# Optimization experiments

Measured on AMD Instinct MI355X. Metric: run time of the kernel, lower is better.

## Reference

```python
import jax, jax.numpy as jnp
import numpy as np

H = 512      # n_lstm_hidden (hardcoded in module)
ATTN = 256   # n_attn_hidden (hardcoded in module)


def setup_inputs() -> dict:
    key = jax.random.key(0)
    ks = jax.random.split(key, 10)
    seq_len, teams, nt = 16, 16, 64
    na = teams * 8
    bs = seq_len * nt
    return {
        "x": jax.random.normal(ks[0], (seq_len, teams, 16), jnp.float32),
        "hxs": jax.random.normal(ks[1], (bs, na, H), jnp.float32),
        "cxs": jax.random.normal(ks[2], (bs, na, H), jnp.float32),
        "h_self": jax.random.normal(ks[3], (bs, na, H), jnp.float32),
        "h_inter": jax.random.normal(ks[4], (bs, na, ATTN), jnp.float32),
        "reset": jax.random.randint(ks[5], (bs, 1), 0, 2, jnp.int32),
        "W_ih": jax.random.normal(ks[6], (4 * H, H), jnp.float32) * 0.02,
        "W_hh": jax.random.normal(ks[7], (4 * H, H), jnp.float32) * 0.02,
        "b_ih": jnp.zeros((4 * H,), jnp.float32),
        "b_hh": jnp.zeros((4 * H,), jnp.float32),
    }


def reference(x, hxs, cxs, h_self, h_inter, reset, W_ih, W_hh, b_ih, b_hh):
    seq_len, teams = x.shape[0], x.shape[1]
    na = teams * 8
    bs = h_self.shape[0]
    nt = bs // seq_len

    # LSTM input: tail half of self features concatenated with inter features -> (bs, na, H)
    h = jnp.concatenate([h_self[:, :, ATTN:], h_inter], axis=-1)
    # (bs, na, H) -> (seq_len, nt*na, H), matching view(nt,seq,na,-1).transpose(1,0)
    h_seq = h.reshape(nt, seq_len, na, H).transpose(1, 0, 2, 3).reshape(seq_len, nt * na, H)

    # per-step keep mask: resets[i::seq_len] == reset.reshape(nt, seq_len)[:, i]
    m = 1.0 - reset.astype(h.dtype).reshape(nt, seq_len).T          # (seq_len, nt)
    m_seq = jnp.broadcast_to(m[:, :, None], (seq_len, nt, na)).reshape(seq_len, nt * na, 1)

    # initial state from each trajectory start: hxs[::seq_len]
    h0 = hxs[::seq_len].reshape(nt * na, H)
    c0 = cxs[::seq_len].reshape(nt * na, H)

    def step(carry, inp):
        hp, cp = carry
        xt, mt = inp
        hp = hp * mt
        cp = cp * mt
        gates = xt @ W_ih.T + b_ih + hp @ W_hh.T + b_hh
        i, f, g, o = jnp.split(gates, 4, axis=-1)
        c = jax.nn.sigmoid(f) * cp + jax.nn.sigmoid(i) * jnp.tanh(g)
        hn = jax.nn.sigmoid(o) * jnp.tanh(c)
        return (hn, c), (hn, c)

    _, (hys, cys) = jax.lax.scan(step, (h0, c0), (h_seq, m_seq))

    def fold(y):
        # (seq_len, nt*na, H) -> transpose to (nt, seq, na, H) contiguous,
        # then torch .view(seq_len, nt, -1) reinterpretation == reshape here
        return y.reshape(seq_len, nt, na, H).transpose(1, 0, 2, 3).reshape(seq_len, nt, na * H)

    hys_out = fold(hys)
    cys_out = fold(cys)
    return (hys_out, cys_out)
```

## Files before the change

kernel.cpp:

```cpp
#include <hip/hip_runtime.h>

typedef __attribute__((ext_vector_type(8))) short bf16x8;
typedef __attribute__((ext_vector_type(16))) float f32x16;

#define SEQ  16
#define NAG  128
#define HD   512

__device__ __forceinline__ unsigned short f2bf(float x) {
  unsigned int u = __float_as_uint(x);
  return (unsigned short)((u + 0x7fffu + ((u >> 16) & 1u)) >> 16);
}
__device__ __forceinline__ float sigm(float x) { return 1.0f / (1.0f + __expf(-x)); }
__device__ __forceinline__ float tanh_(float x) { return 2.0f / (1.0f + __expf(-2.0f * x)) - 1.0f; }

__global__ void prep_pack(const float* __restrict__ Wih, const float* __restrict__ Whh,
                          const float* __restrict__ bih, const float* __restrict__ bhh,
                          unsigned short* __restrict__ Wpk, float* __restrict__ bsum) {
  const int t  = blockIdx.x >> 6;
  const int ks = blockIdx.x & 63;
  const int l  = threadIdx.x;
  const int n  = t * 32 + (l & 31);
  const int k  = ks * 16 + (l >> 5) * 8;
  const float* p = (k < 512) ? (Wih + (size_t)n * 512 + k) : (Whh + (size_t)n * 512 + (k - 512));
  float4 w0 = *reinterpret_cast<const float4*>(p);
  float4 w1 = *reinterpret_cast<const float4*>(p + 4);
  bf16x8 v = {(short)f2bf(w0.x), (short)f2bf(w0.y), (short)f2bf(w0.z), (short)f2bf(w0.w),
              (short)f2bf(w1.x), (short)f2bf(w1.y), (short)f2bf(w1.z), (short)f2bf(w1.w)};
  *reinterpret_cast<bf16x8*>(Wpk + ((size_t)blockIdx.x * 64 + l) * 8) = v;
  if (ks == 0 && l < 32) bsum[n] = bih[n] + bhh[n];
}

template <bool PACKED>
__device__ __forceinline__ bf16x8 loadB(const unsigned short* __restrict__ Wpk,
                                        const float* __restrict__ Wih,
                                        const float* __restrict__ Whh,
                                        int tile, int ks, int lane) {
  if (PACKED) {
    return *reinterpret_cast<const bf16x8*>(Wpk + (((size_t)tile * 64 + ks) * 64 + lane) * 8);
  } else {
    int n = tile * 32 + (lane & 31);
    int k = ks * 16 + (lane >> 5) * 8;
    const float* p = (k < 512) ? (Wih + (size_t)n * 512 + k) : (Whh + (size_t)n * 512 + (k - 512));
    float4 w0 = *reinterpret_cast<const float4*>(p);
    float4 w1 = *reinterpret_cast<const float4*>(p + 4);
    return bf16x8{(short)f2bf(w0.x), (short)f2bf(w0.y), (short)f2bf(w0.z), (short)f2bf(w0.w),
                  (short)f2bf(w1.x), (short)f2bf(w1.y), (short)f2bf(w1.z), (short)f2bf(w1.w)};
  }
}

template <bool PACKED>
__global__ __launch_bounds__(512, 2)
void lstm32(const float* __restrict__ hxs, const float* __restrict__ cxs,
            const float* __restrict__ h_self, const float* __restrict__ h_inter,
            const int* __restrict__ reset,
            const unsigned short* __restrict__ Wpk, const float* __restrict__ bsum,
            const float* __restrict__ Wih, const float* __restrict__ Whh,
            const float* __restrict__ bih, const float* __restrict__ bhh,
            float* __restrict__ out) {
  __shared__ __align__(16) unsigned short x_lds[32 * 512];
  __shared__ __align__(16) unsigned short h_lds[2][32 * 512];

  const int tid  = threadIdx.x;
  const int w    = tid >> 6;
  const int lane = tid & 63;
  const int colB = lane & 31;
  const int khB  = lane >> 5;
  const int row  = colB;
  const int asw  = (row & 7) << 3;

  const int bid    = blockIdx.x;
  const int traj   = bid >> 2;
  const int agent0 = (bid & 3) * 32;

  const int rS  = tid >> 4;
  const int l16 = tid & 15;
  const int swS = (rS & 7) << 3;

  const size_t CYS = (size_t)SEQ * 64 * NAG * HD;

  {
    const float* src = hxs + ((size_t)traj * SEQ * NAG + (agent0 + rS)) * HD;
    #pragma unroll
    for (int p = 0; p < 8; ++p) {
      int k = p * 64 + l16 * 4;
      float4 v = *reinterpret_cast<const float4*>(src + k);
      ushort4 u4 = make_ushort4(f2bf(v.x), f2bf(v.y), f2bf(v.z), f2bf(v.w));
      *reinterpret_cast<ushort4*>(&h_lds[0][rS * 512 + (k ^ swS)]) = u4;
    }
  }

  float c_reg[2][16];
  float biasv[2][4];
  {
    #pragma unroll
    for (int u = 0; u < 2; ++u)
      #pragma unroll
      for (int q = 0; q < 4; ++q) {
        int n = q * 512 + w * 64 + u * 32 + colB;
        biasv[u][q] = PACKED ? bsum[n] : (bih[n] + bhh[n]);
      }
    const size_t cbase = ((size_t)traj * SEQ * NAG + agent0) * HD;
    #pragma unroll
    for (int u = 0; u < 2; ++u)
      #pragma unroll
      for (int reg = 0; reg < 16; ++reg) {
        int r  = (reg & 3) + 8 * (reg >> 2) + 4 * khB;
        int hd = w * 64 + u * 32 + colB;
        c_reg[u][reg] = cxs[cbase + (size_t)r * HD + hd];
      }
  }

  for (int t = 0; t < SEQ; ++t) {
    const int b  = traj * SEQ + t;
    const int mt = 1 - reset[b];
    const unsigned short* hcur = h_lds[t & 1];
    unsigned short*       hnxt = h_lds[(t & 1) ^ 1];

    {
      const float* srcs = h_self  + ((size_t)b * NAG + (agent0 + rS)) * HD + 256;
      const float* srci = h_inter + ((size_t)b * NAG + (agent0 + rS)) * 256;
      #pragma unroll
      for (int p = 0; p < 8; ++p) {
        int k = p * 64 + l16 * 4;
        const float* sp = (k < 256) ? (srcs + k) : (srci + (k - 256));
        float4 v = *reinterpret_cast<const float4*>(sp);
        ushort4 u4 = make_ushort4(f2bf(v.x), f2bf(v.y), f2bf(v.z), f2bf(v.w));
        *reinterpret_cast<ushort4*>(&x_lds[rS * 512 + (k ^ swS)]) = u4;
      }
      if (mt == 0) {
        uint4* pz = (uint4*)h_lds[t & 1];
        #pragma unroll
        for (int i = 0; i < 4; ++i) pz[tid + i * 512] = uint4{0, 0, 0, 0};
      }
    }
    __syncthreads();

    auto lda = [&](int ks) -> bf16x8 {
      int kk = (ks & 31) * 16 + khB * 8;
      const unsigned short* src = (ks < 32) ? x_lds : hcur;
      return *reinterpret_cast<const bf16x8*>(src + row * 512 + (kk ^ asw));
    };

    #pragma unroll
    for (int u = 0; u < 2; ++u) {
      const int t0 = 0 * 16 + w * 2 + u, t1 = 1 * 16 + w * 2 + u,
                t2 = 2 * 16 + w * 2 + u, t3 = 3 * 16 + w * 2 + u;
      f32x16 acc[4];
      #pragma unroll
      for (int q = 0; q < 4; ++q)
        #pragma unroll
        for (int e = 0; e < 16; ++e) acc[q][e] = 0.0f;

      bf16x8 Ba[4], Bb[4];
      Ba[0] = loadB<PACKED>(Wpk, Wih, Whh, t0, 0, lane);
      Ba[1] = loadB<PACKED>(Wpk, Wih, Whh, t1, 0, lane);
      Ba[2] = loadB<PACKED>(Wpk, Wih, Whh, t2, 0, lane);
      Ba[3] = loadB<PACKED>(Wpk, Wih, Whh, t3, 0, lane);
      Bb[0] = loadB<PACKED>(Wpk, Wih, Whh, t0, 1, lane);
      Bb[1] = loadB<PACKED>(Wpk, Wih, Whh, t1, 1, lane);
      Bb[2] = loadB<PACKED>(Wpk, Wih, Whh, t2, 1, lane);
      Bb[3] = loadB<PACKED>(Wpk, Wih, Whh, t3, 1, lane);

      #pragma unroll 1
      for (int kp = 0; kp < 32; ++kp) {
        const int ks0 = kp * 2;
        bf16x8 a0 = lda(ks0);
        __builtin_amdgcn_s_setprio(1);
        acc[0] = __builtin_amdgcn_mfma_f32_32x32x16_bf16(a0, Ba[0], acc[0], 0, 0, 0);
        acc[1] = __builtin_amdgcn_mfma_f32_32x32x16_bf16(a0, Ba[1], acc[1], 0, 0, 0);
        acc[2] = __builtin_amdgcn_mfma_f32_32x32x16_bf16(a0, Ba[2], acc[2], 0, 0, 0);
        acc[3] = __builtin_amdgcn_mfma_f32_32x32x16_bf16(a0, Ba[3], acc[3], 0, 0, 0);
        __builtin_amdgcn_s_setprio(0);
        const int ksn0 = (ks0 + 2 < 64) ? ks0 + 2 : 63;
        Ba[0] = loadB<PACKED>(Wpk, Wih, Whh, t0, ksn0, lane);
        Ba[1] = loadB<PACKED>(Wpk, Wih, Whh, t1, ksn0, lane);
        Ba[2] = loadB<PACKED>(Wpk, Wih, Whh, t2, ksn0, lane);
        Ba[3] = loadB<PACKED>(Wpk, Wih, Whh, t3, ksn0, lane);
        bf16x8 a1 = lda(ks0 + 1);
        __builtin_amdgcn_s_setprio(1);
        acc[0] = __builtin_amdgcn_mfma_f32_32x32x16_bf16(a1, Bb[0], acc[0], 0, 0, 0);
        acc[1] = __builtin_amdgcn_mfma_f32_32x32x16_bf16(a1, Bb[1], acc[1], 0, 0, 0);
        acc[2] = __builtin_amdgcn_mfma_f32_32x32x16_bf16(a1, Bb[2], acc[2], 0, 0, 0);
        acc[3] = __builtin_amdgcn_mfma_f32_32x32x16_bf16(a1, Bb[3], acc[3], 0, 0, 0);
        __builtin_amdgcn_s_setprio(0);
        const int ksn1 = (ks0 + 3 < 64) ? ks0 + 3 : 63;
        Bb[0] = loadB<PACKED>(Wpk, Wih, Whh, t0, ksn1, lane);
        Bb[1] = loadB<PACKED>(Wpk, Wih, Whh, t1, ksn1, lane);
        Bb[2] = loadB<PACKED>(Wpk, Wih, Whh, t2, ksn1, lane);
        Bb[3] = loadB<PACKED>(Wpk, Wih, Whh, t3, ksn1, lane);
      }

      const int hd = w * 64 + u * 32 + colB;
      #pragma unroll
      for (int reg = 0; reg < 16; ++reg) {
        float gi = acc[0][reg] + biasv[u][0];
        float gf = acc[1][reg] + biasv[u][1];
        float gg = acc[2][reg] + biasv[u][2];
        float go = acc[3][reg] + biasv[u][3];
        float cp = mt ? c_reg[u][reg] : 0.0f;
        float cn = sigm(gf) * cp + sigm(gi) * tanh_(gg);
        float hn = sigm(go) * tanh_(cn);
        c_reg[u][reg] = cn;
        int r = (reg & 3) + 8 * (reg >> 2) + 4 * khB;
        size_t ob = ((size_t)b * NAG + agent0 + r) * HD + hd;
        out[ob] = hn;
        out[CYS + ob] = cn;
        hnxt[r * 512 + (hd ^ ((r & 7) << 3))] = f2bf(hn);
      }
    }
    __syncthreads();
  }
}

extern "C" void kernel_launch(void* const* d_in, const int* in_sizes, int n_in,
                              void* d_out, int out_size, void* d_ws, size_t ws_size,
                              hipStream_t stream) {
  (void)in_sizes; (void)n_in; (void)out_size;
  const float* hxs     = (const float*)d_in[1];
  const float* cxs     = (const float*)d_in[2];
  const float* h_self  = (const float*)d_in[3];
  const float* h_inter = (const float*)d_in[4];
  const int*   reset   = (const int*)d_in[5];
  const float* Wih     = (const float*)d_in[6];
  const float* Whh     = (const float*)d_in[7];
  const float* bih     = (const float*)d_in[8];
  const float* bhh     = (const float*)d_in[9];
  float* out = (float*)d_out;

  const size_t needW = (size_t)2048 * 1024 * sizeof(unsigned short);
  const size_t need  = needW + 2048 * sizeof(float);

  if (d_ws != nullptr && ws_size >= need) {
    unsigned short* Wpk = (unsigned short*)d_ws;
    float* bsum = (float*)((char*)d_ws + needW);
    prep_pack<<<4096, 64, 0, stream>>>(Wih, Whh, bih, bhh, Wpk, bsum);
    lstm32<true><<<256, 512, 0, stream>>>(hxs, cxs, h_self, h_inter, reset,
                                          Wpk, bsum, Wih, Whh, bih, bhh, out);
  } else {
    lstm32<false><<<256, 512, 0, stream>>>(hxs, cxs, h_self, h_inter, reset,
                                           nullptr, nullptr, Wih, Whh, bih, bhh, out);
  }
}
```

Baseline: 998.4 us.

## Double block to 16 waves, each owning one column tile per gate

Blocks grow from 512 to 1024 threads. Each of 16 waves now computes one 32-column tile for all four gates, instead of 8 waves each looping over two tiles. The bias is folded into the accumulator initialisation, and the LDS swizzle is widened to cover all 32 rows. This halves the serial MFMA chain per wave and adds more waves to hide weight-load latency, at the cost of register pressure from the aggressive launch bounds hint.

```diff
diff --git a/kernel.cpp b/kernel.cpp
--- a/kernel.cpp
+++ b/kernel.cpp
@@ -3,9 +3,9 @@
 typedef __attribute__((ext_vector_type(8))) short bf16x8;
 typedef __attribute__((ext_vector_type(16))) float f32x16;
 
-#define SEQ  16
-#define NAG  128
-#define HD   512
+#define SEQ 16
+#define NAG 128
+#define HD  512
 
 __device__ __forceinline__ unsigned short f2bf(float x) {
   unsigned int u = __float_as_uint(x);
@@ -32,32 +32,27 @@
 }
 
 template <bool PACKED>
-__device__ __forceinline__ bf16x8 loadB(const unsigned short* __restrict__ Wpk,
-                                        const float* __restrict__ Wih,
-                                        const float* __restrict__ Whh,
-                                        int tile, int ks, int lane) {
-  if (PACKED) {
-    return *reinterpret_cast<const bf16x8*>(Wpk + (((size_t)tile * 64 + ks) * 64 + lane) * 8);
-  } else {
-    int n = tile * 32 + (lane & 31);
-    int k = ks * 16 + (lane >> 5) * 8;
-    const float* p = (k < 512) ? (Wih + (size_t)n * 512 + k) : (Whh + (size_t)n * 512 + (k - 512));
-    float4 w0 = *reinterpret_cast<const float4*>(p);
-    float4 w1 = *reinterpret_cast<const float4*>(p + 4);
-    return bf16x8{(short)f2bf(w0.x), (short)f2bf(w0.y), (short)f2bf(w0.z), (short)f2bf(w0.w),
-                  (short)f2bf(w1.x), (short)f2bf(w1.y), (short)f2bf(w1.z), (short)f2bf(w1.w)};
-  }
+__device__ __forceinline__ bf16x8 loadBf(const float* __restrict__ Wih,
+                                         const float* __restrict__ Whh,
+                                         int tile, int ks, int lane) {
+  int n = tile * 32 + (lane & 31);
+  int k = ks * 16 + (lane >> 5) * 8;
+  const float* p = (k < 512) ? (Wih + (size_t)n * 512 + k) : (Whh + (size_t)n * 512 + (k - 512));
+  float4 w0 = *reinterpret_cast<const float4*>(p);
+  float4 w1 = *reinterpret_cast<const float4*>(p + 4);
+  return bf16x8{(short)f2bf(w0.x), (short)f2bf(w0.y), (short)f2bf(w0.z), (short)f2bf(w0.w),
+                (short)f2bf(w1.x), (short)f2bf(w1.y), (short)f2bf(w1.z), (short)f2bf(w1.w)};
 }
 
 template <bool PACKED>
-__global__ __launch_bounds__(512, 2)
-void lstm32(const float* __restrict__ hxs, const float* __restrict__ cxs,
-            const float* __restrict__ h_self, const float* __restrict__ h_inter,
-            const int* __restrict__ reset,
-            const unsigned short* __restrict__ Wpk, const float* __restrict__ bsum,
-            const float* __restrict__ Wih, const float* __restrict__ Whh,
-            const float* __restrict__ bih, const float* __restrict__ bhh,
-            float* __restrict__ out) {
+__global__ __launch_bounds__(1024, 4)
+void lstm16w(const float* __restrict__ hxs, const float* __restrict__ cxs,
+             const float* __restrict__ h_self, const float* __restrict__ h_inter,
+             const int* __restrict__ reset,
+             const unsigned short* __restrict__ Wpk, const float* __restrict__ bsum,
+             const float* __restrict__ Wih, const float* __restrict__ Whh,
+             const float* __restrict__ bih, const float* __restrict__ bhh,
+             float* __restrict__ out) {
   __shared__ __align__(16) unsigned short x_lds[32 * 512];
   __shared__ __align__(16) unsigned short h_lds[2][32 * 512];
 
@@ -67,49 +62,47 @@
   const int colB = lane & 31;
   const int khB  = lane >> 5;
   const int row  = colB;
-  const int asw  = (row & 7) << 3;
 
   const int bid    = blockIdx.x;
   const int traj   = bid >> 2;
   const int agent0 = (bid & 3) * 32;
 
-  const int rS  = tid >> 4;
-  const int l16 = tid & 15;
-  const int swS = (rS & 7) << 3;
+  const int rS  = tid >> 5;
+  const int l32 = tid & 31;
+  const int swS = (rS & 31) << 3;
 
   const size_t CYS = (size_t)SEQ * 64 * NAG * HD;
 
   {
     const float* src = hxs + ((size_t)traj * SEQ * NAG + (agent0 + rS)) * HD;
     #pragma unroll
-    for (int p = 0; p < 8; ++p) {
-      int k = p * 64 + l16 * 4;
+    for (int p = 0; p < 4; ++p) {
+      int k = p * 128 + l32 * 4;
       float4 v = *reinterpret_cast<const float4*>(src + k);
       ushort4 u4 = make_ushort4(f2bf(v.x), f2bf(v.y), f2bf(v.z), f2bf(v.w));
       *reinterpret_cast<ushort4*>(&h_lds[0][rS * 512 + (k ^ swS)]) = u4;
     }
   }
 
-  float c_reg[2][16];
-  float biasv[2][4];
+  const int hd = w * 32 + colB;
+  float c_reg[16];
+  float biasv[4];
   {
     #pragma unroll
-    for (int u = 0; u < 2; ++u)
-      #pragma unroll
-      for (int q = 0; q < 4; ++q) {
-        int n = q * 512 + w * 64 + u * 32 + colB;
-        biasv[u][q] = PACKED ? bsum[n] : (bih[n] + bhh[n]);
-      }
+    for (int q = 0; q < 4; ++q)
+      biasv[q] = PACKED ? bsum[q * 512 + hd] : (bih[q * 512 + hd] + bhh[q * 512 + hd]);
     const size_t cbase = ((size_t)traj * SEQ * NAG + agent0) * HD;
     #pragma unroll
-    for (int u = 0; u < 2; ++u)
-      #pragma unroll
-      for (int reg = 0; reg < 16; ++reg) {
-        int r  = (reg & 3) + 8 * (reg >> 2) + 4 * khB;
-        int hd = w * 64 + u * 32 + colB;
-        c_reg[u][reg] = cxs[cbase + (size_t)r * HD + hd];
-      }
-  }
+    for (int reg = 0; reg < 16; ++reg) {
+      int r = (reg & 3) + 8 * (reg >> 2) + 4 * khB;
+      c_reg[reg] = cxs[cbase + (size_t)r * HD + hd];
+    }
+  }
+
+  const unsigned short* Wt0 = Wpk + ((size_t)(0 * 16 + w)) * 64 * 64 * 8;
+  const unsigned short* Wt1 = Wpk + ((size_t)(1 * 16 + w)) * 64 * 64 * 8;
+  const unsigned short* Wt2 = Wpk + ((size_t)(2 * 16 + w)) * 64 * 64 * 8;
+  const unsigned short* Wt3 = Wpk + ((size_t)(3 * 16 + w)) * 64 * 64 * 8;
 
   for (int t = 0; t < SEQ; ++t) {
     const int b  = traj * SEQ + t;
@@ -121,8 +114,8 @@
       const float* srcs = h_self  + ((size_t)b * NAG + (agent0 + rS)) * HD + 256;
       const float* srci = h_inter + ((size_t)b * NAG + (agent0 + rS)) * 256;
       #pragma unroll
-      for (int p = 0; p < 8; ++p) {
-        int k = p * 64 + l16 * 4;
+      for (int p = 0; p < 4; ++p) {
+        int k = p * 128 + l32 * 4;
         const float* sp = (k < 256) ? (srcs + k) : (srci + (k - 256));
         float4 v = *reinterpret_cast<const float4*>(sp);
         ushort4 u4 = make_ushort4(f2bf(v.x), f2bf(v.y), f2bf(v.z), f2bf(v.w));
@@ -130,84 +123,84 @@
       }
       if (mt == 0) {
         uint4* pz = (uint4*)h_lds[t & 1];
-        #pragma unroll
-        for (int i = 0; i < 4; ++i) pz[tid + i * 512] = uint4{0, 0, 0, 0};
+        pz[tid] = uint4{0, 0, 0, 0};
+        pz[tid + 1024] = uint4{0, 0, 0, 0};
       }
     }
     __syncthreads();
 
-    auto lda = [&](int ks) -> bf16x8 {
-      int kk = (ks & 31) * 16 + khB * 8;
-      const unsigned short* src = (ks < 32) ? x_lds : hcur;
-      return *reinterpret_cast<const bf16x8*>(src + row * 512 + (kk ^ asw));
+    f32x16 acc[4];
+    #pragma unroll
+    for (int q = 0; q < 4; ++q)
+      #pragma unroll
+      for (int e = 0; e < 16; ++e) acc[q][e] = biasv[q];
+
+    bf16x8 B0[4], B1[4];
+    auto ldB = [&](bf16x8* B, int ks) {
+      if (PACKED) {
+        const int off = (ks * 64 + lane) * 8;
+        B[0] = *reinterpret_cast<const bf16x8*>(Wt0 + off);
+        B[1] = *reinterpret_cast<const bf16x8*>(Wt1 + off);
+        B[2] = *reinterpret_cast<const bf16x8*>(Wt2 + off);
+        B[3] = *reinterpret_cast<const bf16x8*>(Wt3 + off);
+      } else {
+        B[0] = loadBf<PACKED>(Wih, Whh, 0 * 16 + w, ks, lane);
+        B[1] = loadBf<PACKED>(Wih, Whh, 1 * 16 + w, ks, lane);
+        B[2] = loadBf<PACKED>(Wih, Whh, 2 * 16 + w, ks, lane);
+        B[3] = loadBf<PACKED>(Wih, Whh, 3 * 16 + w, ks, lane);
+      }
     };
-
-    #pragma unroll
-    for (int u = 0; u < 2; ++u) {
-      const int t0 = 0 * 16 + w * 2 + u, t1 = 1 * 16 + w * 2 + u,
-                t2 = 2 * 16 + w * 2 + u, t3 = 3 * 16 + w * 2 + u;
-      f32x16 acc[4];
-      #pragma unroll
-      for (int q = 0; q < 4; ++q)
-        #pragma unroll
-        for (int e = 0; e < 16; ++e) acc[q][e] = 0.0f;
-
-      bf16x8 Ba[4], Bb[4];
-      Ba[0] = loadB<PACKED>(Wpk, Wih, Whh, t0, 0, lane);
-      Ba[1] = loadB<PACKED>(Wpk, Wih, Whh, t1, 0, lane);
-      Ba[2] = loadB<PACKED>(Wpk, Wih, Whh, t2, 0, lane);
-      Ba[3] = loadB<PACKED>(Wpk, Wih, Whh, t3, 0, lane);
-      Bb[0] = loadB<PACKED>(Wpk, Wih, Whh, t0, 1, lane);
-      Bb[1] = loadB<PACKED>(Wpk, Wih, Whh, t1, 1, lane);
-      Bb[2] = loadB<PACKED>(Wpk, Wih, Whh, t2, 1, lane);
-      Bb[3] = loadB<PACKED>(Wpk, Wih, Whh, t3, 1, lane);
-
-      #pragma unroll 1
-      for (int kp = 0; kp < 32; ++kp) {
-        const int ks0 = kp * 2;
-        bf16x8 a0 = lda(ks0);
+    ldB(B0, 0);
+    ldB(B1, 1);
+
+    auto body = [&](int kp, const unsigned short* abuf) {
+      const int ks0 = kp * 2;
+      {
+        const int ea = (((ks0 & 31) * 16 + khB * 8) ^ (row << 3));
+        bf16x8 a = *reinterpret_cast<const bf16x8*>(abuf + row * 512 + ea);
         __builtin_amdgcn_s_setprio(1);
-        acc[0] = __builtin_amdgcn_mfma_f32_32x32x16_bf16(a0, Ba[0], acc[0], 0, 0, 0);
-        acc[1] = __builtin_amdgcn_mfma_f32_32x32x16_bf16(a0, Ba[1], acc[1], 0, 0, 0);
-        acc[2] = __builtin_amdgcn_mfma_f32_32x32x16_bf16(a0, Ba[2], acc[2], 0, 0, 0);
-        acc[3] = __builtin_amdgcn_mfma_f32_32x32x16_bf16(a0, Ba[3], acc[3], 0, 0, 0);
+        acc[0] = __builtin_amdgcn_mfma_f32_32x32x16_bf16(a, B0[0], acc[0], 0, 0, 0);
+        acc[1] = __builtin_amdgcn_mfma_f32_32x32x16_bf16(a, B0[1], acc[1], 0, 0, 0);
+        acc[2] = __builtin_amdgcn_mfma_f32_32x32x16_bf16(a, B0[2], acc[2], 0, 0, 0);
+        acc[3] = __builtin_amdgcn_mfma_f32_32x32x16_bf16(a, B0[3], acc[3], 0, 0, 0);
         __builtin_amdgcn_s_setprio(0);
-        const int ksn0 = (ks0 + 2 < 64) ? ks0 + 2 : 63;
-        Ba[0] = loadB<PACKED>(Wpk, Wih, Whh, t0, ksn0, lane);
-        Ba[1] = loadB<PACKED>(Wpk, Wih, Whh, t1, ksn0, lane);
-        Ba[2] = loadB<PACKED>(Wpk, Wih, Whh, t2, ksn0, lane);
-        Ba[3] = loadB<PACKED>(Wpk, Wih, Whh, t3, ksn0, lane);
-        bf16x8 a1 = lda(ks0 + 1);
+        const int kn = (ks0 + 2 < 64) ? ks0 + 2 : 63;
+        ldB(B0, kn);
+      }
+      {
+        const int ea = ((((ks0 + 1) & 31) * 16 + khB * 8) ^ (row << 3));
+        bf16x8 a = *reinterpret_cast<const bf16x8*>(abuf + row * 512 + ea);
         __builtin_amdgcn_s_setprio(1);
-        acc[0] = __builtin_amdgcn_mfma_f32_32x32x16_bf16(a1, Bb[0], acc[0], 0, 0, 0);
-        acc[1] = __builtin_amdgcn_mfma_f32_32x32x16_bf16(a1, Bb[1], acc[1], 0, 0, 0);
-        acc[2] = __builtin_amdgcn_mfma_f32_32x32x16_bf16(a1, Bb[2], acc[2], 0, 0, 0);
-        acc[3] = __builtin_amdgcn_mfma_f32_32x32x16_bf16(a1, Bb[3], acc[3], 0, 0, 0);
+        acc[0] = __builtin_amdgcn_mfma_f32_32x32x16_bf16(a, B1[0], acc[0], 0, 0, 0);
+        acc[1] = __builtin_amdgcn_mfma_f32_32x32x16_bf16(a, B1[1], acc[1], 0, 0, 0);
+        acc[2] = __builtin_amdgcn_mfma_f32_32x32x16_bf16(a, B1[2], acc[2], 0, 0, 0);
+        acc[3] = __builtin_amdgcn_mfma_f32_32x32x16_bf16(a, B1[3], acc[3], 0, 0, 0);
         __builtin_amdgcn_s_setprio(0);
-        const int ksn1 = (ks0 + 3 < 64) ? ks0 + 3 : 63;
-        Bb[0] = loadB<PACKED>(Wpk, Wih, Whh, t0, ksn1, lane);
-        Bb[1] = loadB<PACKED>(Wpk, Wih, Whh, t1, ksn1, lane);
-        Bb[2] = loadB<PACKED>(Wpk, Wih, Whh, t2, ksn1, lane);
-        Bb[3] = loadB<PACKED>(Wpk, Wih, Whh, t3, ksn1, lane);
-      }
-
-      const int hd = w * 64 + u * 32 + colB;
-      #pragma unroll
-      for (int reg = 0; reg < 16; ++reg) {
-        float gi = acc[0][reg] + biasv[u][0];
-        float gf = acc[1][reg] + biasv[u][1];
-        float gg = acc[2][reg] + biasv[u][2];
-        float go = acc[3][reg] + biasv[u][3];
-        float cp = mt ? c_reg[u][reg] : 0.0f;
-        float cn = sigm(gf) * cp + sigm(gi) * tanh_(gg);
-        float hn = sigm(go) * tanh_(cn);
-        c_reg[u][reg] = cn;
-        int r = (reg & 3) + 8 * (reg >> 2) + 4 * khB;
-        size_t ob = ((size_t)b * NAG + agent0 + r) * HD + hd;
-        out[ob] = hn;
-        out[CYS + ob] = cn;
-        hnxt[r * 512 + (hd ^ ((r & 7) << 3))] = f2bf(hn);
-      }
+        const int kn = (ks0 + 3 < 64) ? ks0 + 3 : 63;
+        ldB(B1, kn);
+      }
+    };
+
+    #pragma unroll 1
+    for (int kp = 0; kp < 16; ++kp) body(kp, x_lds);
+    #pragma unroll 1
+    for (int kp = 16; kp < 32; ++kp) body(kp, hcur);
+
+    #pragma unroll
+    for (int reg = 0; reg < 16; ++reg) {
+      float gi = acc[0][reg];
+      float gf = acc[1][reg];
+      float gg = acc[2][reg];
+      float go = acc[3][reg];
+      float cp = mt ? c_reg[reg] : 0.0f;
+      float cn = sigm(gf) * cp + sigm(gi) * tanh_(gg);
+      float hn = sigm(go) * tanh_(cn);
+      c_reg[reg] = cn;
+      int r = (reg & 3) + 8 * (reg >> 2) + 4 * khB;
+      size_t ob = ((size_t)b * NAG + agent0 + r) * HD + hd;
+      out[ob] = hn;
+      out[CYS + ob] = cn;
+      hnxt[r * 512 + (hd ^ (r << 3))] = f2bf(hn);
     }
     __syncthreads();
   }
@@ -235,10 +228,10 @@
     unsigned short* Wpk = (unsigned short*)d_ws;
     float* bsum = (float*)((char*)d_ws + needW);
     prep_pack<<<4096, 64, 0, stream>>>(Wih, Whh, bih, bhh, Wpk, bsum);
-    lstm32<true><<<256, 512, 0, stream>>>(hxs, cxs, h_self, h_inter, reset,
-                                          Wpk, bsum, Wih, Whh, bih, bhh, out);
+    lstm16w<true><<<256, 1024, 0, stream>>>(hxs, cxs, h_self, h_inter, reset,
+                                            Wpk, bsum, Wih, Whh, bih, bhh, out);
   } else {
-    lstm32<false><<<256, 512, 0, stream>>>(hxs, cxs, h_self, h_inter, reset,
-                                           nullptr, nullptr, Wih, Whh, bih, bhh, out);
-  }
-}
+    lstm16w<false><<<256, 1024, 0, stream>>>(hxs, cxs, h_self, h_inter, reset,
+                                             nullptr, nullptr, Wih, Whh, bih, bhh, out);
+  }
+}
```

After: 1.202 ms. 20.4% more time.

## Deepen weight prefetch to eight k-steps and widen LDS swizzle

Applied to the files above, without the earlier changes.

The GEMM inner loop now keeps eight k-steps of B fragments in registers, up from two, so global weight loads have more MFMA work to hide behind. The k loop is split into x and h phases so the A source is known at compile time. The bias is folded into the accumulator initialisation. The LDS XOR swizzle is widened from 8 to 32 rows to reduce bank conflicts. The extra 32 bf16x8 registers per thread raise register pressure and may cause spills under the 2-blocks-per-CU launch bound.

```diff
diff --git a/kernel.cpp b/kernel.cpp
--- a/kernel.cpp
+++ b/kernel.cpp
@@ -3,9 +3,9 @@
 typedef __attribute__((ext_vector_type(8))) short bf16x8;
 typedef __attribute__((ext_vector_type(16))) float f32x16;
 
-#define SEQ  16
-#define NAG  128
-#define HD   512
+#define SEQ 16
+#define NAG 128
+#define HD  512
 
 __device__ __forceinline__ unsigned short f2bf(float x) {
   unsigned int u = __float_as_uint(x);
@@ -14,50 +14,45 @@
 __device__ __forceinline__ float sigm(float x) { return 1.0f / (1.0f + __expf(-x)); }
 __device__ __forceinline__ float tanh_(float x) { return 2.0f / (1.0f + __expf(-2.0f * x)) - 1.0f; }
 
-__global__ void prep_pack(const float* __restrict__ Wih, const float* __restrict__ Whh,
-                          const float* __restrict__ bih, const float* __restrict__ bhh,
-                          unsigned short* __restrict__ Wpk, float* __restrict__ bsum) {
+__global__ void prep_pack32(const float* __restrict__ Wih, const float* __restrict__ Whh,
+                            const float* __restrict__ bih, const float* __restrict__ bhh,
+                            unsigned short* __restrict__ Wpk, float* __restrict__ bsum) {
   const int t  = blockIdx.x >> 6;
   const int ks = blockIdx.x & 63;
   const int l  = threadIdx.x;
   const int n  = t * 32 + (l & 31);
   const int k  = ks * 16 + (l >> 5) * 8;
   const float* p = (k < 512) ? (Wih + (size_t)n * 512 + k) : (Whh + (size_t)n * 512 + (k - 512));
-  float4 w0 = *reinterpret_cast<const float4*>(p);
-  float4 w1 = *reinterpret_cast<const float4*>(p + 4);
+  float4 w0 = *(const float4*)p;
+  float4 w1 = *(const float4*)(p + 4);
   bf16x8 v = {(short)f2bf(w0.x), (short)f2bf(w0.y), (short)f2bf(w0.z), (short)f2bf(w0.w),
               (short)f2bf(w1.x), (short)f2bf(w1.y), (short)f2bf(w1.z), (short)f2bf(w1.w)};
-  *reinterpret_cast<bf16x8*>(Wpk + ((size_t)blockIdx.x * 64 + l) * 8) = v;
+  *(bf16x8*)(Wpk + ((size_t)blockIdx.x * 64 + l) * 8) = v;
   if (ks == 0 && l < 32) bsum[n] = bih[n] + bhh[n];
 }
 
 template <bool PACKED>
-__device__ __forceinline__ bf16x8 loadB(const unsigned short* __restrict__ Wpk,
-                                        const float* __restrict__ Wih,
-                                        const float* __restrict__ Whh,
-                                        int tile, int ks, int lane) {
-  if (PACKED) {
-    return *reinterpret_cast<const bf16x8*>(Wpk + (((size_t)tile * 64 + ks) * 64 + lane) * 8);
-  } else {
-    int n = tile * 32 + (lane & 31);
-    int k = ks * 16 + (lane >> 5) * 8;
-    const float* p = (k < 512) ? (Wih + (size_t)n * 512 + k) : (Whh + (size_t)n * 512 + (k - 512));
-    float4 w0 = *reinterpret_cast<const float4*>(p);
-    float4 w1 = *reinterpret_cast<const float4*>(p + 4);
-    return bf16x8{(short)f2bf(w0.x), (short)f2bf(w0.y), (short)f2bf(w0.z), (short)f2bf(w0.w),
-                  (short)f2bf(w1.x), (short)f2bf(w1.y), (short)f2bf(w1.z), (short)f2bf(w1.w)};
-  }
+__device__ __forceinline__ bf16x8 loadBf(const float* __restrict__ Wih,
+                                         const float* __restrict__ Whh,
+                                         int tile, int ks, int lane) {
+  int n = tile * 32 + (lane & 31);
+  int k = ks * 16 + (lane >> 5) * 8;
+  const float* p = (k < 512) ? (Wih + (size_t)n * 512 + k) : (Whh + (size_t)n * 512 + (k - 512));
+  float4 w0 = *(const float4*)p;
+  float4 w1 = *(const float4*)(p + 4);
+  return bf16x8{(short)f2bf(w0.x), (short)f2bf(w0.y), (short)f2bf(w0.z), (short)f2bf(w0.w),
+                (short)f2bf(w1.x), (short)f2bf(w1.y), (short)f2bf(w1.z), (short)f2bf(w1.w)};
 }
 
 template <bool PACKED>
 __global__ __launch_bounds__(512, 2)
-void lstm32(const float* __restrict__ hxs, const float* __restrict__ cxs,
-            const float* __restrict__ h_self, const float* __restrict__ h_inter,
-            const int* __restrict__ reset,
-            const unsigned short* __restrict__ Wpk, const float* __restrict__ bsum,
-            const float* __restrict__ Wih, const float* __restrict__ Whh,
-            const float* __restrict__ bih, const float* __restrict__ bhh,
-            float* __restrict__ out) {
+void lstm_d8(const float* __restrict__ hxs, const float* __restrict__ cxs,
+             const float* __restrict__ h_self, const float* __restrict__ h_inter,
+             const int* __restrict__ reset,
+             const unsigned short* __restrict__ Wpk, const float* __restrict__ bsum,
+             const float* __restrict__ Wih, const float* __restrict__ Whh,
+             const float* __restrict__ bih, const float* __restrict__ bhh,
+             float* __restrict__ out) {
   __shared__ __align__(16) unsigned short x_lds[32 * 512];
   __shared__ __align__(16) unsigned short h_lds[2][32 * 512];
 
@@ -67,16 +62,11 @@
   const int colB = lane & 31;
   const int khB  = lane >> 5;
   const int row  = colB;
-  const int asw  = (row & 7) << 3;
-
-  const int bid    = blockIdx.x;
-  const int traj   = bid >> 2;
-  const int agent0 = (bid & 3) * 32;
-
-  const int rS  = tid >> 4;
-  const int l16 = tid & 15;
-  const int swS = (rS & 7) << 3;
-
+  const int asw  = (row & 31) << 3;
+
+  const int bid = blockIdx.x, traj = bid >> 2, agent0 = (bid & 3) * 32;
+  const int rS = tid >> 4, l16 = tid & 15;
+  const int swS = (rS & 31) << 3;
   const size_t CYS = (size_t)SEQ * 64 * NAG * HD;
 
   {
@@ -84,9 +74,9 @@
     #pragma unroll
     for (int p = 0; p < 8; ++p) {
       int k = p * 64 + l16 * 4;
-      float4 v = *reinterpret_cast<const float4*>(src + k);
-      ushort4 u4 = make_ushort4(f2bf(v.x), f2bf(v.y), f2bf(v.z), f2bf(v.w));
-      *reinterpret_cast<ushort4*>(&h_lds[0][rS * 512 + (k ^ swS)]) = u4;
+      float4 v = *(const float4*)(src + k);
+      *(ushort4*)&h_lds[0][rS * 512 + (k ^ swS)] =
+          make_ushort4(f2bf(v.x), f2bf(v.y), f2bf(v.z), f2bf(v.w));
     }
   }
 
@@ -105,9 +95,8 @@
     for (int u = 0; u < 2; ++u)
       #pragma unroll
       for (int reg = 0; reg < 16; ++reg) {
-        int r  = (reg & 3) + 8 * (reg >> 2) + 4 * khB;
-        int hd = w * 64 + u * 32 + colB;
-        c_reg[u][reg] = cxs[cbase + (size_t)r * HD + hd];
+        int r = (reg & 3) + 8 * (reg >> 2) + 4 * khB;
+        c_reg[u][reg] = cxs[cbase + (size_t)r * HD + w * 64 + u * 32 + colB];
       }
   }
 
@@ -124,9 +113,9 @@
       for (int p = 0; p < 8; ++p) {
         int k = p * 64 + l16 * 4;
         const float* sp = (k < 256) ? (srcs + k) : (srci + (k - 256));
-        float4 v = *reinterpret_cast<const float4*>(sp);
-        ushort4 u4 = make_ushort4(f2bf(v.x), f2bf(v.y), f2bf(v.z), f2bf(v.w));
-        *reinterpret_cast<ushort4*>(&x_lds[rS * 512 + (k ^ swS)]) = u4;
+        float4 v = *(const float4*)sp;
+        *(ushort4*)&x_lds[rS * 512 + (k ^ swS)] =
+            make_ushort4(f2bf(v.x), f2bf(v.y), f2bf(v.z), f2bf(v.w));
       }
       if (mt == 0) {
         uint4* pz = (uint4*)h_lds[t & 1];
@@ -136,68 +125,85 @@
     }
     __syncthreads();
 
-    auto lda = [&](int ks) -> bf16x8 {
+    auto lda = [&](int ks, const unsigned short* src) -> bf16x8 {
       int kk = (ks & 31) * 16 + khB * 8;
-      const unsigned short* src = (ks < 32) ? x_lds : hcur;
-      return *reinterpret_cast<const bf16x8*>(src + row * 512 + (kk ^ asw));
+      return *(const bf16x8*)(src + row * 512 + (kk ^ asw));
     };
 
     #pragma unroll
     for (int u = 0; u < 2; ++u) {
-      const int t0 = 0 * 16 + w * 2 + u, t1 = 1 * 16 + w * 2 + u,
-                t2 = 2 * 16 + w * 2 + u, t3 = 3 * 16 + w * 2 + u;
+      const int t0 = w * 2 + u, t1 = 16 + w * 2 + u, t2 = 32 + w * 2 + u, t3 = 48 + w * 2 + u;
       f32x16 acc[4];
       #pragma unroll
       for (int q = 0; q < 4; ++q)
         #pragma unroll
-        for (int e = 0; e < 16; ++e) acc[q][e] = 0.0f;
-
-      bf16x8 Ba[4], Bb[4];
-      Ba[0] = loadB<PACKED>(Wpk, Wih, Whh, t0, 0, lane);
-      Ba[1] = loadB<PACKED>(Wpk, Wih, Whh, t1, 0, lane);
-      Ba[2] = loadB<PACKED>(Wpk, Wih, Whh, t2, 0, lane);
-      Ba[3] = loadB<PACKED>(Wpk, Wih, Whh, t3, 0, lane);
-      Bb[0] = loadB<PACKED>(Wpk, Wih, Whh, t0, 1, lane);
-      Bb[1] = loadB<PACKED>(Wpk, Wih, Whh, t1, 1, lane);
-      Bb[2] = loadB<PACKED>(Wpk, Wih, Whh, t2, 1, lane);
-      Bb[3] = loadB<PACKED>(Wpk, Wih, Whh, t3, 1, lane);
+        for (int e = 0; e < 16; ++e) acc[q][e] = biasv[u][q];
+
+      bf16x8 Bq[8][4];
+      auto ldB = [&](bf16x8* B, int ks) {
+        if (PACKED) {
+          const size_t off = ((size_t)ks * 64 + lane) * 8;
+          B[0] = *(const bf16x8*)(Wpk + (size_t)t0 * 32768 + off);
+          B[1] = *(const bf16x8*)(Wpk + (size_t)t1 * 32768 + off);
+          B[2] = *(const bf16x8*)(Wpk + (size_t)t2 * 32768 + off);
+          B[3] = *(const bf16x8*)(Wpk + (size_t)t3 * 32768 + off);
+        } else {
+          B[0] = loadBf<PACKED>(Wih, Whh, t0, ks, lane);
+          B[1] = loadBf<PACKED>(Wih, Whh, t1, ks, lane);
+          B[2] = loadBf<PACKED>(Wih, Whh, t2, ks, lane);
+          B[3] = loadBf<PACKED>(Wih, Whh, t3, ks, lane);
+        }
+      };
+
+      #pragma unroll
+      for (int d = 0; d < 8; ++d) ldB(Bq[d], d);
 
       #pragma unroll 1
-      for (int kp = 0; kp < 32; ++kp) {
-        const int ks0 = kp * 2;
-        bf16x8 a0 = lda(ks0);
+      for (int kp = 0; kp < 4; ++kp) {
+        #pragma unroll
+        for (int d = 0; d < 8; ++d) {
+          const int ks = kp * 8 + d;
+          bf16x8 a = lda(ks, x_lds);
+          __builtin_amdgcn_s_setprio(1);
+          acc[0] = __builtin_amdgcn_mfma_f32_32x32x16_bf16(a, Bq[d][0], acc[0], 0, 0, 0);
+          acc[1] = __builtin_amdgcn_mfma_f32_32x32x16_bf16(a, Bq[d][1], acc[1], 0, 0, 0);
+          acc[2] = __builtin_amdgcn_mfma_f32_32x32x16_bf16(a, Bq[d][2], acc[2], 0, 0, 0);
+          acc[3] = __builtin_amdgcn_mfma_f32_32x32x16_bf16(a, Bq[d][3], acc[3], 0, 0, 0);
+          __builtin_amdgcn_s_setprio(0);
+          ldB(Bq[d], ks + 8);
+        }
+      }
+      #pragma unroll 1
+      for (int kp = 0; kp < 3; ++kp) {
+        #pragma unroll
+        for (int d = 0; d < 8; ++d) {
+          const int ks = 32 + kp * 8 + d;
+          bf16x8 a = lda(ks, hcur);
+          __builtin_amdgcn_s_setprio(1);
+          acc[0] = __builtin_amdgcn_mfma_f32_32x32x16_bf16(a, Bq[d][0], acc[0], 0, 0, 0);
+          acc[1] = __builtin_amdgcn_mfma_f32_32x32x16_bf16(a, Bq[d][1], acc[1], 0, 0, 0);
+          acc[2] = __builtin_amdgcn_mfma_f32_32x32x16_bf16(a, Bq[d][2], acc[2], 0, 0, 0);
+          acc[3] = __builtin_amdgcn_mfma_f32_32x32x16_bf16(a, Bq[d][3], acc[3], 0, 0, 0);
+          __builtin_amdgcn_s_setprio(0);
+          ldB(Bq[d], ks + 8);
+        }
+      }
+      #pragma unroll
+      for (int d = 0; d < 8; ++d) {
+        const int ks = 56 + d;
+        bf16x8 a = lda(ks, hcur);
         __builtin_amdgcn_s_setprio(1);
-        acc[0] = __builtin_amdgcn_mfma_f32_32x32x16_bf16(a0, Ba[0], acc[0], 0, 0, 0);
-        acc[1] = __builtin_amdgcn_mfma_f32_32x32x16_bf16(a0, Ba[1], acc[1], 0, 0, 0);
-        acc[2] = __builtin_amdgcn_mfma_f32_32x32x16_bf16(a0, Ba[2], acc[2], 0, 0, 0);
-        acc[3] = __builtin_amdgcn_mfma_f32_32x32x16_bf16(a0, Ba[3], acc[3], 0, 0, 0);
+        acc[0] = __builtin_amdgcn_mfma_f32_32x32x16_bf16(a, Bq[d][0], acc[0], 0, 0, 0);
+        acc[1] = __builtin_amdgcn_mfma_f32_32x32x16_bf16(a, Bq[d][1], acc[1], 0, 0, 0);
+        acc[2] = __builtin_amdgcn_mfma_f32_32x32x16_bf16(a, Bq[d][2], acc[2], 0, 0, 0);
+        acc[3] = __builtin_amdgcn_mfma_f32_32x32x16_bf16(a, Bq[d][3], acc[3], 0, 0, 0);
         __builtin_amdgcn_s_setprio(0);
-        const int ksn0 = (ks0 + 2 < 64) ? ks0 + 2 : 63;
-        Ba[0] = loadB<PACKED>(Wpk, Wih, Whh, t0, ksn0, lane);
-        Ba[1] = loadB<PACKED>(Wpk, Wih, Whh, t1, ksn0, lane);
-        Ba[2] = loadB<PACKED>(Wpk, Wih, Whh, t2, ksn0, lane);
-        Ba[3] = loadB<PACKED>(Wpk, Wih, Whh, t3, ksn0, lane);
-        bf16x8 a1 = lda(ks0 + 1);
-        __builtin_amdgcn_s_setprio(1);
-        acc[0] = __builtin_amdgcn_mfma_f32_32x32x16_bf16(a1, Bb[0], acc[0], 0, 0, 0);
-        acc[1] = __builtin_amdgcn_mfma_f32_32x32x16_bf16(a1, Bb[1], acc[1], 0, 0, 0);
-        acc[2] = __builtin_amdgcn_mfma_f32_32x32x16_bf16(a1, Bb[2], acc[2], 0, 0, 0);
-        acc[3] = __builtin_amdgcn_mfma_f32_32x32x16_bf16(a1, Bb[3], acc[3], 0, 0, 0);
-        __builtin_amdgcn_s_setprio(0);
-        const int ksn1 = (ks0 + 3 < 64) ? ks0 + 3 : 63;
-        Bb[0] = loadB<PACKED>(Wpk, Wih, Whh, t0, ksn1, lane);
-        Bb[1] = loadB<PACKED>(Wpk, Wih, Whh, t1, ksn1, lane);
-        Bb[2] = loadB<PACKED>(Wpk, Wih, Whh, t2, ksn1, lane);
-        Bb[3] = loadB<PACKED>(Wpk, Wih, Whh, t3, ksn1, lane);
       }
 
       const int hd = w * 64 + u * 32 + colB;
       #pragma unroll
       for (int reg = 0; reg < 16; ++reg) {
-        float gi = acc[0][reg] + biasv[u][0];
-        float gf = acc[1][reg] + biasv[u][1];
-        float gg = acc[2][reg] + biasv[u][2];
-        float go = acc[3][reg] + biasv[u][3];
+        float gi = acc[0][reg], gf = acc[1][reg], gg = acc[2][reg], go = acc[3][reg];
         float cp = mt ? c_reg[u][reg] : 0.0f;
         float cn = sigm(gf) * cp + sigm(gi) * tanh_(gg);
         float hn = sigm(go) * tanh_(cn);
@@ -206,7 +212,7 @@
         size_t ob = ((size_t)b * NAG + agent0 + r) * HD + hd;
         out[ob] = hn;
         out[CYS + ob] = cn;
-        hnxt[r * 512 + (hd ^ ((r & 7) << 3))] = f2bf(hn);
+        hnxt[r * 512 + (hd ^ ((r & 31) << 3))] = f2bf(hn);
       }
     }
     __syncthreads();
@@ -229,16 +235,16 @@
   float* out = (float*)d_out;
 
   const size_t needW = (size_t)2048 * 1024 * sizeof(unsigned short);
-  const size_t need  = needW + 2048 * sizeof(float);
+  const size_t need  = needW + 8192;
 
   if (d_ws != nullptr && ws_size >= need) {
-    unsigned short* Wpk = (unsigned short*)d_ws;
-    float* bsum = (float*)((char*)d_ws + needW);
-    prep_pack<<<4096, 64, 0, stream>>>(Wih, Whh, bih, bhh, Wpk, bsum);
-    lstm32<true><<<256, 512, 0, stream>>>(hxs, cxs, h_self, h_inter, reset,
-                                          Wpk, bsum, Wih, Whh, bih, bhh, out);
+    unsigned short* Wpk  = (unsigned short*)d_ws;
+    float*          bsum = (float*)((char*)d_ws + needW);
+    prep_pack32<<<4096, 64, 0, stream>>>(Wih, Whh, bih, bhh, Wpk, bsum);
+    lstm_d8<true><<<256, 512, 0, stream>>>(hxs, cxs, h_self, h_inter, reset,
+                                           Wpk, bsum, Wih, Whh, bih, bhh, out);
   } else {
-    lstm32<false><<<256, 512, 0, stream>>>(hxs, cxs, h_self, h_inter, reset,
-                                           nullptr, nullptr, Wih, Whh, bih, bhh, out);
-  }
-}
+    lstm_d8<false><<<256, 512, 0, stream>>>(hxs, cxs, h_self, h_inter, reset,
+                                            nullptr, nullptr, Wih, Whh, bih, bhh, out);
+  }
+}
```

Result: slower. 1.943 ms (+94.6%).
